# Kernel tuning notes

Measured on AMD Instinct MI355X. Metric: run time of the kernel, lower is better.

Reference implementation:

```python
import jax, jax.numpy as jnp
from jax import lax
import numpy as np

H = 64  # hidden_dim


def _lstm_dir(x, W_ih, W_hh, b, reverse):
    # x: [B,T,I]; W_ih: [4H,I]; W_hh: [4H,H]; b: [4H] (b_ih+b_hh combined)
    B = x.shape[0]
    xp = jnp.einsum('bti,gi->btg', x, W_ih) + b          # [B,T,4H]
    xp = jnp.swapaxes(xp, 0, 1)                          # [T,B,4H]

    def step(carry, xt):
        h, c = carry
        g = xt + h @ W_hh.T                              # [B,4H]
        i, f, gg, o = jnp.split(g, 4, axis=-1)           # PyTorch gate order i,f,g,o
        i = jax.nn.sigmoid(i)
        f = jax.nn.sigmoid(f)
        gg = jnp.tanh(gg)
        o = jax.nn.sigmoid(o)
        c = f * c + i * gg
        h = o * jnp.tanh(c)
        return (h, c), h

    init = (jnp.zeros((B, H), x.dtype), jnp.zeros((B, H), x.dtype))
    _, hs = lax.scan(step, init, xp, reverse=reverse)    # outputs aligned to original positions
    return jnp.swapaxes(hs, 0, 1)                        # [B,T,H]


def _bilstm_layer(x, Wih_f, Whh_f, b_f, Wih_b, Whh_b, b_b):
    fwd = _lstm_dir(x, Wih_f, Whh_f, b_f, reverse=False)
    bwd = _lstm_dir(x, Wih_b, Whh_b, b_b, reverse=True)
    return jnp.concatenate([fwd, bwd], axis=-1)          # [B,T,2H]


def setup_inputs() -> dict:
    key = jax.random.key(0)
    ks = jax.random.split(key, 16)
    s = 0.1
    d = {}
    d['x'] = jax.random.normal(ks[0], (512, 512, 4), dtype=jnp.float32)
    # layer 0 (input size 4), forward / backward directions
    d['Wih_l0_f'] = jax.random.normal(ks[1], (4 * H, 4)) * s
    d['Whh_l0_f'] = jax.random.normal(ks[2], (4 * H, H)) * s
    d['b_l0_f'] = jax.random.normal(ks[3], (4 * H,)) * s
    d['Wih_l0_b'] = jax.random.normal(ks[4], (4 * H, 4)) * s
    d['Whh_l0_b'] = jax.random.normal(ks[5], (4 * H, H)) * s
    d['b_l0_b'] = jax.random.normal(ks[6], (4 * H,)) * s
    # layer 1 (input size 2H = 128)
    d['Wih_l1_f'] = jax.random.normal(ks[7], (4 * H, 2 * H)) * s
    d['Whh_l1_f'] = jax.random.normal(ks[8], (4 * H, H)) * s
    d['b_l1_f'] = jax.random.normal(ks[9], (4 * H,)) * s
    d['Wih_l1_b'] = jax.random.normal(ks[10], (4 * H, 2 * H)) * s
    d['Whh_l1_b'] = jax.random.normal(ks[11], (4 * H, H)) * s
    d['b_l1_b'] = jax.random.normal(ks[12], (4 * H,)) * s
    # final linear: 2H -> 1
    d['fc_w'] = jax.random.normal(ks[13], (1, 2 * H)) * s
    d['fc_b'] = jax.random.normal(ks[14], (1,)) * s
    return d


def reference(x, Wih_l0_f, Whh_l0_f, b_l0_f, Wih_l0_b, Whh_l0_b, b_l0_b,
              Wih_l1_f, Whh_l1_f, b_l1_f, Wih_l1_b, Whh_l1_b, b_l1_b,
              fc_w, fc_b):
    h0 = _bilstm_layer(x, Wih_l0_f, Whh_l0_f, b_l0_f, Wih_l0_b, Whh_l0_b, b_l0_b)
    h1 = _bilstm_layer(h0, Wih_l1_f, Whh_l1_f, b_l1_f, Wih_l1_b, Whh_l1_b, b_l1_b)
    pooled = jnp.mean(h1, axis=1)                        # [B,2H]
    return pooled @ fc_w.T + fc_b                        # [B,1]
```

## Files before the change

### kernel.cpp

```cpp
#include <hip/hip_runtime.h>

#define H  64
#define TT 512
#define BB 512
#define CSTR 80
#define UCH 16
#define XROW 264
#define XCH  (UCH * XROW + 8)
#define NCHUNK (TT / UCH)

typedef _Float16 half8 __attribute__((ext_vector_type(8)));
typedef float    f32x4 __attribute__((ext_vector_type(4)));

#define LOG2E 1.4426950408889634f
#define TWOL  2.8853900817779268f
#define FOURL 5.7707801635558536f

#define MFMA16 __builtin_amdgcn_mfma_f32_16x16x32_f16

__device__ __forceinline__ float frcp(float x) { return __builtin_amdgcn_rcpf(x); }
__device__ __forceinline__ float ex2(float x)  { return __builtin_amdgcn_exp2f(x); }

__device__ __forceinline__ void step_barrier() {
    asm volatile("s_waitcnt lgkmcnt(0)\n\ts_barrier" ::: "memory");
}

__device__ __forceinline__ float sel4(f32x4 v, bool lo, bool hi) {
    float a = lo ? v[1] : v[0];
    float b = lo ? v[3] : v[2];
    return hi ? b : a;
}

#define L0_ACT()                                                                \
    float e_i = frcp(1.f + ex2(gi));                                            \
    float e_f = frcp(1.f + ex2(gf));                                            \
    float tg  = TWOL - FOURL * frcp(1.f + ex2(gg));                             \
    float e_o = frcp(1.f + ex2(go));                                            \
    cp = e_f * cp + e_i * tg;                                                   \
    float r = frcp(1.f + ex2(cp));                                              \
    float hh = e_o * fmaf(-2.f, r, 1.f);

#define L1_ACT()                                                                \
    float I = ex2(gi), Fv = ex2(gf), G = ex2(gg), O = ex2(go);                  \
    float i1 = 1.f + I;                                                         \
    float rIG = frcp(fmaf(i1, G, i1));                                          \
    float P   = fmaf(TWOL, G, -TWOL) * rIG;           \
    cp = fmaf(frcp(1.f + Fv), cp, P);                                           \
    float Cx = ex2(cp);                                                         \
    float o1 = 1.f + O;                                                         \
    float rOC = frcp(fmaf(o1, Cx, o1));                                         \
    float hh = (Cx - 1.f) * rOC;

__global__ __launch_bounds__(256) void xpad_prep(const float* __restrict__ x,
                                                 _Float16* __restrict__ xpad) {
    int gid = blockIdx.x * 256 + threadIdx.x;
    int row = gid >> 2, q = gid & 3;
    half8 v = {0,0,0,0,0,0,0,0};
    if (q == 0) {
        float4 xv = ((const float4*)x)[row];
        v[0] = (_Float16)xv.x; v[1] = (_Float16)xv.y;
        v[2] = (_Float16)xv.z; v[3] = (_Float16)xv.w;
    }
    *(half8*)(xpad + (size_t)row * 32 + q * 8) = v;
}


#define L0_CHUNK(CIDX, XPR, XPW, AUSE, ALOAD)                                   \
    {                                                                           \
        const int c_ = (CIDX);                                                  \
        if (c_ + 2 < NCHUNK) {                                                  \
            const int tL = dir ? (TT - 1 - ((c_ + 2) * UCH + m))                \
                               : ((c_ + 2) * UCH + m);                          \
            _Pragma("unroll")                                                   \
            for (int cc = 0; cc < 4; ++cc)                                      \
                ALOAD[cc] = *(const half8*)(xpad +                              \
                    (size_t)((b0 + cc) * TT + tL) * 32 + q * 8);                \
        }                                                                       \
        _Pragma("unroll")                                                       \
        for (int u = 0; u < UCH; ++u) {                                         \
            half8 ah0 = *(const half8*)&hbuf[p][ch][q * 8];                     \
            half8 ah1 = *(const half8*)&hbuf[p][ch][32 + q * 8];                \
            f32x4 xq = *(const f32x4*)&XPR[ch * XCH + u * XROW + uo * 4];       \
            f32x4 g0 = MFMA16(Ah[0][0], ah0, vz, 0, 0, 0);                      \
            g0       = MFMA16(Ah[0][1], ah1, g0, 0, 0, 0);                      \
            f32x4 g1 = MFMA16(Ah[1][0], ah0, vz, 0, 0, 0);                      \
            g1       = MFMA16(Ah[1][1], ah1, g1, 0, 0, 0);                      \
            f32x4 g2 = MFMA16(Ah[2][0], ah0, vz, 0, 0, 0);                      \
            g2       = MFMA16(Ah[2][1], ah1, g2, 0, 0, 0);                      \
            f32x4 g3 = MFMA16(Ah[3][0], ah0, vz, 0, 0, 0);                      \
            g3       = MFMA16(Ah[3][1], ah1, g3, 0, 0, 0);                      \
            {                                \
                f32x4 acc = bb[u & 3];                                          \
                acc = MFMA16(Wg[u & 3], AUSE[u >> 2], acc, 0, 0, 0);            \
                *(f32x4*)&XPW[(u >> 2) * XCH + m * XROW +                       \
                              (w * 16 + (u & 3) * 4 + q) * 4] = acc;            \
            }                                                                   \
            float gi = sel4(g0, sLo, sHi) + xq[0];                              \
            float gf = sel4(g1, sLo, sHi) + xq[1];                              \
            float gg = sel4(g2, sLo, sHi) + xq[2];                              \
            float go = sel4(g3, sLo, sHi) + xq[3];                              \
            L0_ACT()                                                            \
            const int tg_t = dir ? (TT - 1 - (c_ * UCH + u)) : (c_ * UCH + u);  \
            out0[((size_t)(b0 + ch) * TT + tg_t) * 128 + dir * 64 + uo] =       \
                (_Float16)hh;                                                   \
            hbuf[p ^ 1][ch][uo] = (_Float16)hh;                                 \
            step_barrier();                                                     \
            p ^= 1;                                                             \
        }                                                                       \
    }

__global__ __launch_bounds__(256, 1) void lstm_l0(
    const _Float16* __restrict__ xpad,
    const float* __restrict__ WihF, const float* __restrict__ WhhF, const float* __restrict__ bF,
    const float* __restrict__ WihB, const float* __restrict__ WhhB, const float* __restrict__ bB,
    _Float16* __restrict__ out0)
{
    const int dir = blockIdx.x & 1;
    const int b0  = (blockIdx.x >> 1) * 4;
    const int tid = threadIdx.x;
    const int w = tid >> 6, l = tid & 63, m = l & 15, q = l >> 4;
    const int ch = m & 3;
    const int i0 = m >> 2;
    const int uo = w * 16 + q * 4 + i0;
    const bool sLo = (i0 & 1) != 0, sHi = (i0 & 2) != 0;

    const float* Wih = dir ? WihB : WihF;
    const float* Whh = dir ? WhhB : WhhF;
    const float* bia = dir ? bB   : bF;

    half8 Ah[4][2];
#pragma unroll
    for (int t = 0; t < 4; ++t) {
        const float st = (t == 2) ? TWOL : -LOG2E;
        const int wrow = t * 64 + w * 16 + m;
#pragma unroll
        for (int s2 = 0; s2 < 2; ++s2) {
            const float* src = Whh + wrow * 64 + s2 * 32 + q * 8;
            half8 tmp;
#pragma unroll
            for (int j = 0; j < 8; ++j) tmp[j] = (_Float16)(src[j] * st);
            Ah[t][s2] = tmp;
        }
    }

    const float sm = ((m & 3) == 2) ? TWOL : -LOG2E;
    half8 Wg[4];
#pragma unroll
    for (int j = 0; j < 4; ++j) {
        const int gr = (m & 3) * 64 + w * 16 + j * 4 + (m >> 2);
        half8 tmp;
#pragma unroll
        for (int jj = 0; jj < 8; ++jj) {
            int k = q * 8 + jj;
            tmp[jj] = (k < 4) ? (_Float16)(Wih[gr * 4 + k] * sm) : (_Float16)0.f;
        }
        Wg[j] = tmp;
    }

    f32x4 bb[4];
#pragma unroll
    for (int j = 0; j < 4; ++j) {
        const int ub = w * 16 + j * 4 + q;
        bb[j][0] = bia[ub]       * -LOG2E;
        bb[j][1] = bia[64 + ub]  * -LOG2E;
        bb[j][2] = bia[128 + ub] * TWOL;
        bb[j][3] = bia[192 + ub] * -LOG2E;
    }

    const f32x4 vz = {0.f, 0.f, 0.f, 0.f};

    __shared__ __align__(16) float xpA[4 * XCH];
    __shared__ __align__(16) float xpB[4 * XCH];
    __shared__ __align__(16) _Float16 hbuf[2][4][CSTR];
    for (int i = tid; i < 2 * 4 * CSTR / 2; i += 256) ((unsigned int*)hbuf)[i] = 0u;

    float cp = 0.f;
    int p = 0;

    half8 aR[2][4];
    {
        const int t0 = dir ? (TT - 1 - m) : m;
        const int t1 = dir ? (TT - 1 - (UCH + m)) : (UCH + m);
#pragma unroll
        for (int cc = 0; cc < 4; ++cc) {
            aR[0][cc] = *(const half8*)(xpad + (size_t)((b0 + cc) * TT + t0) * 32 + q * 8);
            aR[1][cc] = *(const half8*)(xpad + (size_t)((b0 + cc) * TT + t1) * 32 + q * 8);
        }
#pragma unroll
        for (int pp = 0; pp < 16; ++pp) {
            const int cc = pp >> 2, j = pp & 3;
            f32x4 acc = bb[j];
            acc = MFMA16(Wg[j], aR[0][cc], acc, 0, 0, 0);
            *(f32x4*)&xpA[cc * XCH + m * XROW + (w * 16 + j * 4 + q) * 4] = acc;
        }
        __syncthreads();
    }

    for (int c = 0; c < NCHUNK; c += 2) {
        L0_CHUNK(c,     xpA, xpB, aR[1], aR[0]);
        L0_CHUNK(c + 1, xpB, xpA, aR[0], aR[1]);
    }
}

#define L1_CHUNK(CIDX, XPR, XPW, AUSE, ALOAD)                                   \
    {                                                                           \
        const int c_ = (CIDX);                                                  \
        if (c_ + 2 < NCHUNK) {                                                  \
            const int tL = dir ? (TT - 1 - ((c_ + 2) * UCH + m))                \
                               : ((c_ + 2) * UCH + m);                          \
            _Pragma("unroll")                                                   \
            for (int cc = 0; cc < 4; ++cc) {                                    \
                const _Float16* arow = out0 +                                   \
                    (size_t)((b0 + cc) * TT + tL) * 128 + q * 8;                \
                _Pragma("unroll")                                               \
                for (int k4 = 0; k4 < 4; ++k4)                                  \
                    ALOAD[cc][k4] = *(const half8*)(arow + k4 * 32);            \
            }                                                                   \
        }                                                                       \
        _Pragma("unroll")                                                       \
        for (int u = 0; u < UCH; ++u) {                                         \
            half8 ah0 = *(const half8*)&hbuf[p][ch][q * 8];                     \
            half8 ah1 = *(const half8*)&hbuf[p][ch][32 + q * 8];                \
            f32x4 xq = *(const f32x4*)&XPR[ch * XCH + u * XROW + uo * 4];       \
            f32x4 g0 = MFMA16(Ah[0][0], ah0, vz, 0, 0, 0);                      \
            g0       = MFMA16(Ah[0][1], ah1, g0, 0, 0, 0);                      \
            f32x4 g1 = MFMA16(Ah[1][0], ah0, vz, 0, 0, 0);                      \
            g1       = MFMA16(Ah[1][1], ah1, g1, 0, 0, 0);                      \
            f32x4 g2 = MFMA16(Ah[2][0], ah0, vz, 0, 0, 0);                      \
            g2       = MFMA16(Ah[2][1], ah1, g2, 0, 0, 0);                      \
            f32x4 g3 = MFMA16(Ah[3][0], ah0, vz, 0, 0, 0);                      \
            g3       = MFMA16(Ah[3][1], ah1, g3, 0, 0, 0);                      \
            {       \
                f32x4 pA = MFMA16(Wg[u & 3][0], AUSE[u >> 2][0], bb[u & 3], 0,0,0); \
                pA       = MFMA16(Wg[u & 3][1], AUSE[u >> 2][1], pA, 0, 0, 0);  \
                f32x4 pB = MFMA16(Wg[u & 3][2], AUSE[u >> 2][2], vz, 0, 0, 0);  \
                pB       = MFMA16(Wg[u & 3][3], AUSE[u >> 2][3], pB, 0, 0, 0);  \
                f32x4 acc = pA + pB;                                            \
                *(f32x4*)&XPW[(u >> 2) * XCH + m * XROW +                       \
                              (w * 16 + (u & 3) * 4 + q) * 4] = acc;            \
            }                                                                   \
            float gi = sel4(g0, sLo, sHi) + xq[0];                              \
            float gf = sel4(g1, sLo, sHi) + xq[1];                              \
            float gg = sel4(g2, sLo, sHi) + xq[2];                              \
            float go = sel4(g3, sLo, sHi) + xq[3];                              \
            L1_ACT()                                                            \
            hs += hh;                                                           \
            hbuf[p ^ 1][ch][uo] = (_Float16)hh;                                 \
            step_barrier();                                                     \
            p ^= 1;                                                             \
        }                                                                       \
    }

__global__ __launch_bounds__(256, 1) void lstm_l1(
    const _Float16* __restrict__ out0,
    const float* __restrict__ WihF, const float* __restrict__ WhhF, const float* __restrict__ bF,
    const float* __restrict__ WihB, const float* __restrict__ WhhB, const float* __restrict__ bB,
    float* __restrict__ pooled)
{
    const int dir = blockIdx.x & 1;
    const int b0  = (blockIdx.x >> 1) * 4;
    const int tid = threadIdx.x;
    const int w = tid >> 6, l = tid & 63, m = l & 15, q = l >> 4;
    const int ch = m & 3;
    const int i0 = m >> 2;
    const int uo = w * 16 + q * 4 + i0;
    const bool sLo = (i0 & 1) != 0, sHi = (i0 & 2) != 0;

    const float* Wih = dir ? WihB : WihF;
    const float* Whh = dir ? WhhB : WhhF;
    const float* bia = dir ? bB   : bF;

    half8 Ah[4][2];
#pragma unroll
    for (int t = 0; t < 4; ++t) {
        const float st = (t == 2) ? TWOL : -LOG2E;
        const int wrow = t * 64 + w * 16 + m;
#pragma unroll
        for (int s2 = 0; s2 < 2; ++s2) {
            const float* src = Whh + wrow * 64 + s2 * 32 + q * 8;
            half8 tmp;
#pragma unroll
            for (int j = 0; j < 8; ++j) tmp[j] = (_Float16)(src[j] * st);
            Ah[t][s2] = tmp;
        }
    }

    const float sm = ((m & 3) == 2) ? TWOL : -LOG2E;
    half8 Wg[4][4];
#pragma unroll
    for (int j = 0; j < 4; ++j) {
        const int gr = (m & 3) * 64 + w * 16 + j * 4 + (m >> 2);
#pragma unroll
        for (int k4 = 0; k4 < 4; ++k4) {
            const float* src = Wih + gr * 128 + k4 * 32 + q * 8;
            half8 tmp;
#pragma unroll
            for (int jj = 0; jj < 8; ++jj) tmp[jj] = (_Float16)(src[jj] * sm);
            Wg[j][k4] = tmp;
        }
    }

    f32x4 bb[4];
#pragma unroll
    for (int j = 0; j < 4; ++j) {
        const int ub = w * 16 + j * 4 + q;
        bb[j][0] = bia[ub]       * -LOG2E;
        bb[j][1] = bia[64 + ub]  * -LOG2E;
        bb[j][2] = bia[128 + ub] * TWOL;
        bb[j][3] = bia[192 + ub] * -LOG2E;
    }

    const f32x4 vz = {0.f, 0.f, 0.f, 0.f};

    __shared__ __align__(16) float xpA[4 * XCH];
    __shared__ __align__(16) float xpB[4 * XCH];
    __shared__ __align__(16) _Float16 hbuf[2][4][CSTR];
    for (int i = tid; i < 2 * 4 * CSTR / 2; i += 256) ((unsigned int*)hbuf)[i] = 0u;

    float cp = 0.f, hs = 0.f;
    int p = 0;

    half8 aR[2][4][4];
    {
        const int t0 = dir ? (TT - 1 - m) : m;
        const int t1 = dir ? (TT - 1 - (UCH + m)) : (UCH + m);
#pragma unroll
        for (int cc = 0; cc < 4; ++cc) {
            const _Float16* r0 = out0 + (size_t)((b0 + cc) * TT + t0) * 128 + q * 8;
            const _Float16* r1 = out0 + (size_t)((b0 + cc) * TT + t1) * 128 + q * 8;
#pragma unroll
            for (int k4 = 0; k4 < 4; ++k4) {
                aR[0][cc][k4] = *(const half8*)(r0 + k4 * 32);
                aR[1][cc][k4] = *(const half8*)(r1 + k4 * 32);
            }
        }
#pragma unroll
        for (int pp = 0; pp < 16; ++pp) {
            const int cc = pp >> 2, j = pp & 3;
            f32x4 acc = MFMA16(Wg[j][0], aR[0][cc][0], bb[j], 0, 0, 0);
            acc = MFMA16(Wg[j][1], aR[0][cc][1], acc, 0, 0, 0);
            acc = MFMA16(Wg[j][2], aR[0][cc][2], acc, 0, 0, 0);
            acc = MFMA16(Wg[j][3], aR[0][cc][3], acc, 0, 0, 0);
            *(f32x4*)&xpA[cc * XCH + m * XROW + (w * 16 + j * 4 + q) * 4] = acc;
        }
        __syncthreads();
    }

    for (int c = 0; c < NCHUNK; c += 2) {
        L1_CHUNK(c,     xpA, xpB, aR[1], aR[0]);
        L1_CHUNK(c + 1, xpB, xpA, aR[0], aR[1]);
    }

    pooled[(size_t)(b0 + ch) * 128 + dir * 64 + uo] = hs;
}

__global__ __launch_bounds__(64) void fc_head(
    const float* __restrict__ pooled,
    const float* __restrict__ fcw, const float* __restrict__ fcb,
    float* __restrict__ out)
{
    const int b = blockIdx.x;
    const int l = threadIdx.x;
    float v = pooled[b * 128 + l] * fcw[l] + pooled[b * 128 + 64 + l] * fcw[64 + l];
#pragma unroll
    for (int o = 32; o > 0; o >>= 1) v += __shfl_down(v, o);
    if (l == 0) out[b] = v * (1.f / (float)TT) + fcb[0];
}

extern "C" void kernel_launch(void* const* d_in, const int* in_sizes, int n_in,
                              void* d_out, int out_size, void* d_ws, size_t ws_size,
                              hipStream_t stream) {
    const float* x       = (const float*)d_in[0];
    const float* Wih_l0f = (const float*)d_in[1];
    const float* Whh_l0f = (const float*)d_in[2];
    const float* b_l0f   = (const float*)d_in[3];
    const float* Wih_l0b = (const float*)d_in[4];
    const float* Whh_l0b = (const float*)d_in[5];
    const float* b_l0b   = (const float*)d_in[6];
    const float* Wih_l1f = (const float*)d_in[7];
    const float* Whh_l1f = (const float*)d_in[8];
    const float* b_l1f   = (const float*)d_in[9];
    const float* Wih_l1b = (const float*)d_in[10];
    const float* Whh_l1b = (const float*)d_in[11];
    const float* b_l1b   = (const float*)d_in[12];
    const float* fcw     = (const float*)d_in[13];
    const float* fcb     = (const float*)d_in[14];

    const size_t o_xpad   = 0;
    const size_t o_out0   = o_xpad + (size_t)BB * TT * 32 * 2;
    const size_t o_pooled = o_out0 + (size_t)BB * TT * 128 * 2;

    _Float16* xpad   = (_Float16*)((char*)d_ws + o_xpad);
    _Float16* out0   = (_Float16*)((char*)d_ws + o_out0);
    float*    pooled = (float*)((char*)d_ws + o_pooled);

    xpad_prep<<<(BB * TT * 4) / 256, 256, 0, stream>>>(x, xpad);
    lstm_l0<<<(BB / 4) * 2, 256, 0, stream>>>(xpad, Wih_l0f, Whh_l0f, b_l0f,
                                              Wih_l0b, Whh_l0b, b_l0b, out0);
    lstm_l1<<<(BB / 4) * 2, 256, 0, stream>>>(out0, Wih_l1f, Whh_l1f, b_l1f,
                                              Wih_l1b, Whh_l1b, b_l1b, pooled);
    fc_head<<<BB, 64, 0, stream>>>(pooled, fcw, fcb, (float*)d_out);
}
```

Before: 408.7 us.

## Fuse x fp16 padding into layer-0 kernel and split recurrent MFMA chains

Removes the separate xpad_prep kernel: layer 0 now loads the fp32 input directly as float4 and converts it to a zero-padded half8 operand in registers. This saves one launch and a round trip through a 16 MB padded fp16 buffer. Both recurrent kernels also stop chaining the two K-halves of each gate MFMA through the accumulator. They issue independent MFMAs and add the results in scalar code, which shortens the dependent MFMA latency on the serial per-timestep path. The cost is extra VALU adds, extra accumulator registers, and some register pressure from holding prefetched float4 values.

```diff
diff --git a/kernel.cpp b/kernel.cpp
--- a/kernel.cpp
+++ b/kernel.cpp
@@ -51,21 +51,8 @@
     float rOC = frcp(fmaf(o1, Cx, o1));                                         \
     float hh = (Cx - 1.f) * rOC;
 
-__global__ __launch_bounds__(256) void xpad_prep(const float* __restrict__ x,
-                                                 _Float16* __restrict__ xpad) {
-    int gid = blockIdx.x * 256 + threadIdx.x;
-    int row = gid >> 2, q = gid & 3;
-    half8 v = {0,0,0,0,0,0,0,0};
-    if (q == 0) {
-        float4 xv = ((const float4*)x)[row];
-        v[0] = (_Float16)xv.x; v[1] = (_Float16)xv.y;
-        v[2] = (_Float16)xv.z; v[3] = (_Float16)xv.w;
-    }
-    *(half8*)(xpad + (size_t)row * 32 + q * 8) = v;
-}
-
-
-#define L0_CHUNK(CIDX, XPR, XPW, AUSE, ALOAD)                                   \
+
+#define L0_CHUNK(CIDX, XPR, XPW, AUSEF, ALOADF)                                 \
     {                                                                           \
         const int c_ = (CIDX);                                                  \
         if (c_ + 2 < NCHUNK) {                                                  \
@@ -73,32 +60,44 @@
                                : ((c_ + 2) * UCH + m);                          \
             _Pragma("unroll")                                                   \
             for (int cc = 0; cc < 4; ++cc)                                      \
-                ALOAD[cc] = *(const half8*)(xpad +                              \
-                    (size_t)((b0 + cc) * TT + tL) * 32 + q * 8);                \
+                ALOADF[cc] = *(const float4*)(xg +                              \
+                    ((size_t)(b0 + cc) * TT + tL) * 4);                         \
+        }                                                                       \
+              \
+              \
+        half8 aU[4];                                                            \
+        _Pragma("unroll")                                                       \
+        for (int cc = 0; cc < 4; ++cc) {                                        \
+            half8 v = {0,0,0,0,0,0,0,0};                                        \
+            if (q == 0) {                                                       \
+                v[0] = (_Float16)AUSEF[cc].x; v[1] = (_Float16)AUSEF[cc].y;     \
+                v[2] = (_Float16)AUSEF[cc].z; v[3] = (_Float16)AUSEF[cc].w;     \
+            }                                                                   \
+            aU[cc] = v;                                                         \
         }                                                                       \
         _Pragma("unroll")                                                       \
         for (int u = 0; u < UCH; ++u) {                                         \
             half8 ah0 = *(const half8*)&hbuf[p][ch][q * 8];                     \
             half8 ah1 = *(const half8*)&hbuf[p][ch][32 + q * 8];                \
             f32x4 xq = *(const f32x4*)&XPR[ch * XCH + u * XROW + uo * 4];       \
-            f32x4 g0 = MFMA16(Ah[0][0], ah0, vz, 0, 0, 0);                      \
-            g0       = MFMA16(Ah[0][1], ah1, g0, 0, 0, 0);                      \
-            f32x4 g1 = MFMA16(Ah[1][0], ah0, vz, 0, 0, 0);                      \
-            g1       = MFMA16(Ah[1][1], ah1, g1, 0, 0, 0);                      \
-            f32x4 g2 = MFMA16(Ah[2][0], ah0, vz, 0, 0, 0);                      \
-            g2       = MFMA16(Ah[2][1], ah1, g2, 0, 0, 0);                      \
-            f32x4 g3 = MFMA16(Ah[3][0], ah0, vz, 0, 0, 0);                      \
-            g3       = MFMA16(Ah[3][1], ah1, g3, 0, 0, 0);                      \
+            f32x4 g0a = MFMA16(Ah[0][0], ah0, vz, 0, 0, 0);                     \
+            f32x4 g0b = MFMA16(Ah[0][1], ah1, vz, 0, 0, 0);                     \
+            f32x4 g1a = MFMA16(Ah[1][0], ah0, vz, 0, 0, 0);                     \
+            f32x4 g1b = MFMA16(Ah[1][1], ah1, vz, 0, 0, 0);                     \
+            f32x4 g2a = MFMA16(Ah[2][0], ah0, vz, 0, 0, 0);                     \
+            f32x4 g2b = MFMA16(Ah[2][1], ah1, vz, 0, 0, 0);                     \
+            f32x4 g3a = MFMA16(Ah[3][0], ah0, vz, 0, 0, 0);                     \
+            f32x4 g3b = MFMA16(Ah[3][1], ah1, vz, 0, 0, 0);                     \
             {                                \
                 f32x4 acc = bb[u & 3];                                          \
-                acc = MFMA16(Wg[u & 3], AUSE[u >> 2], acc, 0, 0, 0);            \
+                acc = MFMA16(Wg[u & 3], aU[u >> 2], acc, 0, 0, 0);              \
                 *(f32x4*)&XPW[(u >> 2) * XCH + m * XROW +                       \
                               (w * 16 + (u & 3) * 4 + q) * 4] = acc;            \
             }                                                                   \
-            float gi = sel4(g0, sLo, sHi) + xq[0];                              \
-            float gf = sel4(g1, sLo, sHi) + xq[1];                              \
-            float gg = sel4(g2, sLo, sHi) + xq[2];                              \
-            float go = sel4(g3, sLo, sHi) + xq[3];                              \
+            float gi = sel4(g0a, sLo, sHi) + sel4(g0b, sLo, sHi) + xq[0];       \
+            float gf = sel4(g1a, sLo, sHi) + sel4(g1b, sLo, sHi) + xq[1];       \
+            float gg = sel4(g2a, sLo, sHi) + sel4(g2b, sLo, sHi) + xq[2];       \
+            float go = sel4(g3a, sLo, sHi) + sel4(g3b, sLo, sHi) + xq[3];       \
             L0_ACT()                                                            \
             const int tg_t = dir ? (TT - 1 - (c_ * UCH + u)) : (c_ * UCH + u);  \
             out0[((size_t)(b0 + ch) * TT + tg_t) * 128 + dir * 64 + uo] =       \
@@ -110,7 +109,7 @@
     }
 
 __global__ __launch_bounds__(256, 1) void lstm_l0(
-    const _Float16* __restrict__ xpad,
+    const float* __restrict__ xg,
     const float* __restrict__ WihF, const float* __restrict__ WhhF, const float* __restrict__ bF,
     const float* __restrict__ WihB, const float* __restrict__ WhhB, const float* __restrict__ bB,
     _Float16* __restrict__ out0)
@@ -177,28 +176,38 @@
     float cp = 0.f;
     int p = 0;
 
-    half8 aR[2][4];
+    float4 aF[2][4];
     {
         const int t0 = dir ? (TT - 1 - m) : m;
         const int t1 = dir ? (TT - 1 - (UCH + m)) : (UCH + m);
 #pragma unroll
         for (int cc = 0; cc < 4; ++cc) {
-            aR[0][cc] = *(const half8*)(xpad + (size_t)((b0 + cc) * TT + t0) * 32 + q * 8);
-            aR[1][cc] = *(const half8*)(xpad + (size_t)((b0 + cc) * TT + t1) * 32 + q * 8);
+            aF[0][cc] = *(const float4*)(xg + ((size_t)(b0 + cc) * TT + t0) * 4);
+            aF[1][cc] = *(const float4*)(xg + ((size_t)(b0 + cc) * TT + t1) * 4);
+        }
+        half8 a0[4];
+#pragma unroll
+        for (int cc = 0; cc < 4; ++cc) {
+            half8 v = {0,0,0,0,0,0,0,0};
+            if (q == 0) {
+                v[0] = (_Float16)aF[0][cc].x; v[1] = (_Float16)aF[0][cc].y;
+                v[2] = (_Float16)aF[0][cc].z; v[3] = (_Float16)aF[0][cc].w;
+            }
+            a0[cc] = v;
         }
 #pragma unroll
         for (int pp = 0; pp < 16; ++pp) {
             const int cc = pp >> 2, j = pp & 3;
             f32x4 acc = bb[j];
-            acc = MFMA16(Wg[j], aR[0][cc], acc, 0, 0, 0);
+            acc = MFMA16(Wg[j], a0[cc], acc, 0, 0, 0);
             *(f32x4*)&xpA[cc * XCH + m * XROW + (w * 16 + j * 4 + q) * 4] = acc;
         }
         __syncthreads();
     }
 
     for (int c = 0; c < NCHUNK; c += 2) {
-        L0_CHUNK(c,     xpA, xpB, aR[1], aR[0]);
-        L0_CHUNK(c + 1, xpB, xpA, aR[0], aR[1]);
+        L0_CHUNK(c,     xpA, xpB, aF[1], aF[0]);
+        L0_CHUNK(c + 1, xpB, xpA, aF[0], aF[1]);
     }
 }
 
@@ -222,14 +231,14 @@
             half8 ah0 = *(const half8*)&hbuf[p][ch][q * 8];                     \
             half8 ah1 = *(const half8*)&hbuf[p][ch][32 + q * 8];                \
             f32x4 xq = *(const f32x4*)&XPR[ch * XCH + u * XROW + uo * 4];       \
-            f32x4 g0 = MFMA16(Ah[0][0], ah0, vz, 0, 0, 0);                      \
-            g0       = MFMA16(Ah[0][1], ah1, g0, 0, 0, 0);                      \
-            f32x4 g1 = MFMA16(Ah[1][0], ah0, vz, 0, 0, 0);                      \
-            g1       = MFMA16(Ah[1][1], ah1, g1, 0, 0, 0);                      \
-            f32x4 g2 = MFMA16(Ah[2][0], ah0, vz, 0, 0, 0);                      \
-            g2       = MFMA16(Ah[2][1], ah1, g2, 0, 0, 0);                      \
-            f32x4 g3 = MFMA16(Ah[3][0], ah0, vz, 0, 0, 0);                      \
-            g3       = MFMA16(Ah[3][1], ah1, g3, 0, 0, 0);                      \
+            f32x4 g0a = MFMA16(Ah[0][0], ah0, vz, 0, 0, 0);                     \
+            f32x4 g0b = MFMA16(Ah[0][1], ah1, vz, 0, 0, 0);                     \
+            f32x4 g1a = MFMA16(Ah[1][0], ah0, vz, 0, 0, 0);                     \
+            f32x4 g1b = MFMA16(Ah[1][1], ah1, vz, 0, 0, 0);                     \
+            f32x4 g2a = MFMA16(Ah[2][0], ah0, vz, 0, 0, 0);                     \
+            f32x4 g2b = MFMA16(Ah[2][1], ah1, vz, 0, 0, 0);                     \
+            f32x4 g3a = MFMA16(Ah[3][0], ah0, vz, 0, 0, 0);                     \
+            f32x4 g3b = MFMA16(Ah[3][1], ah1, vz, 0, 0, 0);                     \
             {       \
                 f32x4 pA = MFMA16(Wg[u & 3][0], AUSE[u >> 2][0], bb[u & 3], 0,0,0); \
                 pA       = MFMA16(Wg[u & 3][1], AUSE[u >> 2][1], pA, 0, 0, 0);  \
@@ -239,10 +248,10 @@
                 *(f32x4*)&XPW[(u >> 2) * XCH + m * XROW +                       \
                               (w * 16 + (u & 3) * 4 + q) * 4] = acc;            \
             }                                                                   \
-            float gi = sel4(g0, sLo, sHi) + xq[0];                              \
-            float gf = sel4(g1, sLo, sHi) + xq[1];                              \
-            float gg = sel4(g2, sLo, sHi) + xq[2];                              \
-            float go = sel4(g3, sLo, sHi) + xq[3];                              \
+            float gi = sel4(g0a, sLo, sHi) + sel4(g0b, sLo, sHi) + xq[0];       \
+            float gf = sel4(g1a, sLo, sHi) + sel4(g1b, sLo, sHi) + xq[1];       \
+            float gg = sel4(g2a, sLo, sHi) + sel4(g2b, sLo, sHi) + xq[2];       \
+            float go = sel4(g3a, sLo, sHi) + sel4(g3b, sLo, sHi) + xq[3];       \
             L1_ACT()                                                            \
             hs += hh;                                                           \
             hbuf[p ^ 1][ch][uo] = (_Float16)hh;                                 \
@@ -386,16 +395,13 @@
     const float* fcw     = (const float*)d_in[13];
     const float* fcb     = (const float*)d_in[14];
 
-    const size_t o_xpad   = 0;
-    const size_t o_out0   = o_xpad + (size_t)BB * TT * 32 * 2;
+    const size_t o_out0   = 0;
     const size_t o_pooled = o_out0 + (size_t)BB * TT * 128 * 2;
 
-    _Float16* xpad   = (_Float16*)((char*)d_ws + o_xpad);
     _Float16* out0   = (_Float16*)((char*)d_ws + o_out0);
     float*    pooled = (float*)((char*)d_ws + o_pooled);
 
-    xpad_prep<<<(BB * TT * 4) / 256, 256, 0, stream>>>(x, xpad);
-    lstm_l0<<<(BB / 4) * 2, 256, 0, stream>>>(xpad, Wih_l0f, Whh_l0f, b_l0f,
+    lstm_l0<<<(BB / 4) * 2, 256, 0, stream>>>(x, Wih_l0f, Whh_l0f, b_l0f,
                                               Wih_l0b, Whh_l0b, b_l0b, out0);
     lstm_l1<<<(BB / 4) * 2, 256, 0, stream>>>(out0, Wih_l1f, Whh_l1f, b_l1f,
                                               Wih_l1b, Whh_l1b, b_l1b, pooled);
```

Result: slower. 481.6 us (+17.8%).
